# Kernel optimization log

Hardware: AMD Instinct MI355X
Metric: run time of the kernel (lower is better)

## Reference

```python
import jax, jax.numpy as jnp
import numpy as np

TEMP = 0.5
LAMDA = 1.0
NUM_SLICE = 64
EPS = 1e-20


def _gaussian_kernel(size=11, sigma=1.5):
    coords = np.arange(size, dtype=np.float64) - (size - 1) / 2.0
    g = np.exp(-(coords ** 2) / (2.0 * sigma ** 2))
    g = g / g.sum()
    return jnp.asarray(g, dtype=jnp.float32)


def _ssim(x, y, data_range=1.0, win_size=11, sigma=1.5):
    # x, y: [B, S, H, W]; treat each slice as an independent 1-channel image.
    B, S, H, W = x.shape
    x4 = x.reshape(B * S, 1, H, W)
    y4 = y.reshape(B * S, 1, H, W)
    g = _gaussian_kernel(win_size, sigma)
    kh = g.reshape(1, 1, win_size, 1)
    kw = g.reshape(1, 1, 1, win_size)
    dn = ('NCHW', 'OIHW', 'NCHW')

    def blur(a):
        a = jax.lax.conv_general_dilated(a, kh, (1, 1), 'VALID', dimension_numbers=dn)
        a = jax.lax.conv_general_dilated(a, kw, (1, 1), 'VALID', dimension_numbers=dn)
        return a

    mu1 = blur(x4)
    mu2 = blur(y4)
    mu1_sq = mu1 * mu1
    mu2_sq = mu2 * mu2
    mu1_mu2 = mu1 * mu2
    sigma1_sq = blur(x4 * x4) - mu1_sq
    sigma2_sq = blur(y4 * y4) - mu2_sq
    sigma12 = blur(x4 * y4) - mu1_mu2
    C1 = (0.01 * data_range) ** 2
    C2 = (0.03 * data_range) ** 2
    ssim_map = ((2.0 * mu1_mu2 + C1) * (2.0 * sigma12 + C2)) / (
        (mu1_sq + mu2_sq + C1) * (sigma1_sq + sigma2_sq + C2))
    return jnp.mean(ssim_map)


def _l1(a, b):
    return jnp.mean(jnp.abs(a - b))


def _cumulative_mips(img_fake, target, gumbel, temp):
    # Growing-window gumbel-softmax MIP, computed in a single O(S) pass.
    # softmax over a prefix window is shift-invariant, so subtract the
    # per-pixel global max over the slice axis for stability, then use cumsums.
    y = img_fake + gumbel
    m = jnp.max(y, axis=1, keepdims=True)
    e = jnp.exp((y - m) / temp)                      # unnormalized softmax weights
    num = jnp.cumsum(e * img_fake, axis=1)
    den = jnp.cumsum(e, axis=1)
    pred_c1 = num / den                              # prefix windows [0:idx+1]
    target_c1 = jax.lax.cummax(target, axis=1)

    ef = jnp.flip(e, axis=1)
    xf = jnp.flip(img_fake, axis=1)
    num2 = jnp.cumsum(ef * xf, axis=1)
    den2 = jnp.cumsum(ef, axis=1)
    pred_c2 = num2 / den2                            # suffix windows [S-1-idx:]
    target_c2 = jax.lax.cummax(jnp.flip(target, axis=1), axis=1)
    return pred_c1, target_c1, pred_c2, target_c2


def _forward(img_fake, target, u_noise):
    gumbel = -jnp.log(-jnp.log(u_noise + EPS) + EPS)
    p1, t1, p2, t2 = _cumulative_mips(img_fake, target, gumbel, TEMP)
    loss_lissim = (_l1(img_fake, target) + 1.0 - _ssim(img_fake, target)) * LAMDA
    loss_mip_c1 = (_l1(p1, t1) + 1.0 - _ssim(p1, t1)) * LAMDA
    loss_mip_c2 = (_l1(p2, t2) + 1.0 - _ssim(p2, t2)) * LAMDA
    return loss_lissim + loss_mip_c1 + loss_mip_c2


def setup_inputs() -> dict:
    key = jax.random.key(0)
    k1, k2, k3 = jax.random.split(key, 3)
    shape = (2, NUM_SLICE, 256, 256)
    img_fake = jax.random.uniform(k1, shape, dtype=jnp.float32)
    target = jax.random.uniform(k2, shape, dtype=jnp.float32)
    u_noise = jax.random.uniform(k3, shape, dtype=jnp.float32)
    return {"img_fake": img_fake, "target": target, "u_noise": u_noise}


def reference(img_fake, target, u_noise):
    return _forward(img_fake, target, u_noise)
```

## Files before the change

kernel.cpp:

```cpp
#include <hip/hip_runtime.h>
#include <cmath>
#include <cstring>

#define NUM_S   64
#define IMG_H   256
#define IMG_W   256
#define HWSZ    (IMG_H*IMG_W)
#define BATCH   2
#define NPIX    (BATCH*HWSZ)
#define NEL     (BATCH*NUM_S*HWSZ)
#define NSLICE  (BATCH*NUM_S)
#define VALID   246
#define EPS_F   1e-20f
#define C1_F    1e-4f
#define C2_F    9e-4f
#define RS      264
#define FS      (16*RS)
#define NSLOT_SCAN 1024
#define NSLOT_ALL  7168
#define PTPAD   1024

typedef __fp16 half8  __attribute__((ext_vector_type(8)));
typedef __fp16 fp16x2 __attribute__((ext_vector_type(2)));
using fragC = __attribute__((ext_vector_type(4))) float;

union H8 { half8 v; short s[8]; int i[4]; };
union PK { fp16x2 v; int i; };

struct GH { short h[11]; };

__device__ inline fp16x2 pkrtz(float a, float b) {
    return __builtin_amdgcn_cvt_pkrtz(a, b);
}
__device__ inline float frcp(float x)  { return __builtin_amdgcn_rcpf(x); }
__device__ inline float flog2(float x) { return __builtin_amdgcn_logf(x); }
__device__ inline float fexp2(float x) { return __builtin_amdgcn_exp2f(x); }

__device__ inline void block_reduce_slot(float v, float* slot) {
    __shared__ float sm[8];
    __syncthreads();
    #pragma unroll
    for (int off = 32; off; off >>= 1) v += __shfl_down(v, off, 64);
    int lane = threadIdx.x & 63, w = threadIdx.x >> 6;
    if (lane == 0) sm[w] = v;
    __syncthreads();
    if (threadIdx.x == 0) {
        float s = 0.f;
        int nw = blockDim.x >> 6;
        for (int i = 0; i < nw; ++i) s += sm[i];
        *slot = s;
    }
}

__global__ __launch_bounds__(256) void scan_kernel(
    const float* __restrict__ img, const float* __restrict__ tgt,
    const float* __restrict__ un,
    uint2* __restrict__ pt0, uint2* __restrict__ pt1, uint2* __restrict__ pt2,
    float* __restrict__ slots, GH gh, unsigned short* __restrict__ bandTbl)
{
    if (blockIdx.x == 0 && threadIdx.x < 64) {
        int q = threadIdx.x >> 4, n = threadIdx.x & 15;
        #pragma unroll
        for (int j = 0; j < 8; ++j) {
            int kk = q * 8 + j - n;
            short hv = 0;
            #pragma unroll
            for (int w = 0; w < 11; ++w) hv = (kk == w) ? gh.h[w] : hv;
            bandTbl[threadIdx.x * 8 + j] = (unsigned short)hv;
        }
    }

    const int HW2 = HWSZ / 2;
    int tid = blockIdx.x * 256 + threadIdx.x;
    bool bwd = tid >= (NPIX / 2);
    int p2 = bwd ? tid - NPIX / 2 : tid;
    int b   = p2 >> 15;
    int hw2 = p2 & (HW2 - 1);
    int idx  = b * (NUM_S * HW2) + hw2 + (bwd ? (NUM_S - 1) * HW2 : 0);
    int step = bwd ? -HW2 : HW2;
    const float2* __restrict__ img2 = (const float2*)img;
    const float2* __restrict__ tgt2 = (const float2*)tgt;
    const float2* __restrict__ un2  = (const float2*)un;

    float num[2] = {0.f, 0.f}, den[2] = {0.f, 0.f}, tm[2] = {-INFINITY, -INFINITY};
    float l1x = 0.f, l1p = 0.f;

    float2 xb[4], ub[4], tb[4];
    #pragma unroll
    for (int j = 0; j < 4; ++j) {
        int id = idx + j * step;
        xb[j] = img2[id]; ub[j] = un2[id]; tb[j] = tgt2[id];
    }

    for (int i = 0; i < NUM_S; i += 4) {
        #pragma unroll
        for (int j = 0; j < 4; ++j) {
            float2 x = xb[j], u = ub[j], t = tb[j];
            if (i + j + 4 < NUM_S) {
                int id = idx + 4 * step;
                xb[j] = img2[id]; ub[j] = un2[id]; tb[j] = tgt2[id];
            }
            float xc[2] = {x.x, x.y}, uc[2] = {u.x, u.y}, tc[2] = {t.x, t.y};
            float p[2];
            #pragma unroll
            for (int c = 0; c < 2; ++c) {
                float w = fmaf(flog2(uc[c] + EPS_F), -0.6931471805599453f, EPS_F);
                float r = frcp(w);
                float e = fexp2(xc[c] * 2.8853900817779268f) * (r * r);
                num[c] = fmaf(e, xc[c], num[c]);
                den[c] += e;
                p[c] = num[c] * frcp(den[c]);
                tm[c] = fmaxf(tm[c], tc[c]);
                if (!bwd) l1x += fabsf(xc[c] - tc[c]);
                l1p += fabsf(p[c] - tm[c]);
            }
            PK k0, k1;
            k0.v = pkrtz(p[0], tm[0]); k1.v = pkrtz(p[1], tm[1]);
            uint2 pv = make_uint2((unsigned)k0.i, (unsigned)k1.i);
            if (!bwd) {
                PK a0, a1;
                a0.v = pkrtz(xc[0], tc[0]); a1.v = pkrtz(xc[1], tc[1]);
                pt0[idx] = make_uint2((unsigned)a0.i, (unsigned)a1.i);
                pt1[idx] = pv;
            } else {
                pt2[idx] = pv;
            }
            idx += step;
        }
    }
    block_reduce_slot(bwd ? 0.f : l1x, &slots[blockIdx.x]);
    block_reduce_slot(l1p, &slots[512 + blockIdx.x]);
}

__global__ __launch_bounds__(256) void ssim_kernel(
    const unsigned* __restrict__ pt0, const unsigned* __restrict__ pt1,
    const unsigned* __restrict__ pt2,
    const int4* __restrict__ bandTbl, float* __restrict__ slots)
{
    __shared__ short Vl[5][FS];
    int pair  = blockIdx.z;
    int yy    = blockIdx.y;
    int bsel  = yy & 1, ss = yy >> 1;
    int sy    = bsel * NUM_S + ((pair == 2) ? ss : (NUM_S - 1 - ss));
    int base  = sy * HWSZ;
    int r0    = blockIdx.x * 16;
    int lane  = threadIdx.x & 63;
    int wid   = threadIdx.x >> 6;
    int q     = lane >> 4;
    int n     = lane & 15;

    const unsigned* __restrict__ pp =
        (pair == 0 ? pt0 : (pair == 1 ? pt1 : pt2)) + base;
    bool clampR = (r0 == 240);
    const fragC zero = {0.f, 0.f, 0.f, 0.f};

    unsigned ld[32];
    {
        int rowbase = r0 + q * 8;
        if (!clampR) {
            const unsigned* pb = pp + rowbase * IMG_W + n;
            #pragma unroll
            for (int it = 0; it < 4; ++it)
                #pragma unroll
                for (int j = 0; j < 8; ++j)
                    ld[it * 8 + j] = pb[j * IMG_W + (wid * 4 + it) * 16];
        } else {
            #pragma unroll
            for (int it = 0; it < 4; ++it)
                #pragma unroll
                for (int j = 0; j < 8; ++j) {
                    int rr = min(rowbase + j, IMG_H - 1);
                    ld[it * 8 + j] = pp[rr * IMG_W + (wid * 4 + it) * 16 + n];
                }
        }
    }
    H8 band;
    *(int4*)band.i = bandTbl[lane];

    for (int d = threadIdx.x; d < 320; d += 256) {
        int f = d >> 6, rm = d & 63, r = rm >> 2, cc = rm & 3;
        ((int*)Vl)[f * 2112 + r * 132 + 128 + cc] = 0;
    }

    #pragma unroll
    for (int it = 0; it < 4; ++it) {
        H8 fX, fY, fXX, fYY, fXY;
        #pragma unroll
        for (int j = 0; j < 4; ++j) {
            unsigned a = ld[it * 8 + 2 * j], b2 = ld[it * 8 + 2 * j + 1];
            fX.i[j] = (int)((a & 0xffffu) | (b2 << 16));
            fY.i[j] = (int)((a >> 16) | (b2 & 0xffff0000u));
        }
        fXX.v = fX.v * fX.v;
        fYY.v = fY.v * fY.v;
        fXY.v = fX.v * fY.v;
        fragC v0 = __builtin_amdgcn_mfma_f32_16x16x32_f16(fX.v,  band.v, zero, 0, 0, 0);
        fragC v1 = __builtin_amdgcn_mfma_f32_16x16x32_f16(fY.v,  band.v, zero, 0, 0, 0);
        fragC v2 = __builtin_amdgcn_mfma_f32_16x16x32_f16(fXX.v, band.v, zero, 0, 0, 0);
        fragC v3 = __builtin_amdgcn_mfma_f32_16x16x32_f16(fYY.v, band.v, zero, 0, 0, 0);
        fragC v4 = __builtin_amdgcn_mfma_f32_16x16x32_f16(fXY.v, band.v, zero, 0, 0, 0);
        int ro = n * RS + (wid * 4 + it) * 16 + q * 4;
        PK pa, pb;
        pa.v = pkrtz(v0[0], v0[1]); pb.v = pkrtz(v0[2], v0[3]);
        *(int2*)&Vl[0][ro] = make_int2(pa.i, pb.i);
        pa.v = pkrtz(v1[0], v1[1]); pb.v = pkrtz(v1[2], v1[3]);
        *(int2*)&Vl[1][ro] = make_int2(pa.i, pb.i);
        pa.v = pkrtz(v2[0], v2[1]); pb.v = pkrtz(v2[2], v2[3]);
        *(int2*)&Vl[2][ro] = make_int2(pa.i, pb.i);
        pa.v = pkrtz(v3[0], v3[1]); pb.v = pkrtz(v3[2], v3[3]);
        *(int2*)&Vl[3][ro] = make_int2(pa.i, pb.i);
        pa.v = pkrtz(v4[0], v4[1]); pb.v = pkrtz(v4[2], v4[3]);
        *(int2*)&Vl[4][ro] = make_int2(pa.i, pb.i);
    }
    __syncthreads();

    float lsum = 0.f;
    for (int it = 0; it < 4; ++it) {
        int c0 = (wid * 4 + it) * 16;
        int so = n * RS + c0 + q * 8;
        so = min(so, FS - 8);
        H8 a0, a1, a2, a3, a4;
        *(int4*)a0.i = *(const int4*)&Vl[0][so];
        *(int4*)a1.i = *(const int4*)&Vl[1][so];
        *(int4*)a2.i = *(const int4*)&Vl[2][so];
        *(int4*)a3.i = *(const int4*)&Vl[3][so];
        *(int4*)a4.i = *(const int4*)&Vl[4][so];
        fragC o0 = __builtin_amdgcn_mfma_f32_16x16x32_f16(a0.v, band.v, zero, 0, 0, 0);
        fragC o1 = __builtin_amdgcn_mfma_f32_16x16x32_f16(a1.v, band.v, zero, 0, 0, 0);
        fragC o2 = __builtin_amdgcn_mfma_f32_16x16x32_f16(a2.v, band.v, zero, 0, 0, 0);
        fragC o3 = __builtin_amdgcn_mfma_f32_16x16x32_f16(a3.v, band.v, zero, 0, 0, 0);
        fragC o4 = __builtin_amdgcn_mfma_f32_16x16x32_f16(a4.v, band.v, zero, 0, 0, 0);
        #pragma unroll
        for (int reg = 0; reg < 4; ++reg) {
            int r = r0 + q * 4 + reg;
            int c = c0 + n;
            if (r < VALID && c < VALID) {
                float m1 = o0[reg], m2 = o1[reg];
                float s11 = o2[reg] - m1 * m1;
                float s22 = o3[reg] - m2 * m2;
                float s12 = o4[reg] - m1 * m2;
                float nv = (2.f * m1 * m2 + C1_F) * (2.f * s12 + C2_F);
                float dv = (m1 * m1 + m2 * m2 + C1_F) * (s11 + s22 + C2_F);
                lsum += nv * frcp(dv);
            }
        }
    }
    block_reduce_slot(lsum,
        &slots[NSLOT_SCAN + pair * 2048 + blockIdx.y * 16 + blockIdx.x]);
}

__global__ void finalize_kernel(const float* __restrict__ slots,
                                float* __restrict__ out) {
    __shared__ double sa[4], sb[4];
    double a = 0.0, bsum = 0.0;
    for (int i = threadIdx.x; i < NSLOT_SCAN; i += 256) a += (double)slots[i];
    for (int i = NSLOT_SCAN + threadIdx.x; i < NSLOT_ALL; i += 256) bsum += (double)slots[i];
    #pragma unroll
    for (int off = 32; off; off >>= 1) {
        a    += __shfl_down(a, off, 64);
        bsum += __shfl_down(bsum, off, 64);
    }
    int lane = threadIdx.x & 63, w = threadIdx.x >> 6;
    if (lane == 0) { sa[w] = a; sb[w] = bsum; }
    __syncthreads();
    if (threadIdx.x == 0) {
        double A = sa[0] + sa[1] + sa[2] + sa[3];
        double B = sb[0] + sb[1] + sb[2] + sb[3];
        out[0] = (float)(3.0 + A / (double)NEL -
                         B / ((double)NSLICE * (double)VALID * (double)VALID));
    }
}

static unsigned short f32_to_f16(float f) {
    unsigned u; memcpy(&u, &f, 4);
    unsigned s = (u >> 16) & 0x8000u;
    int e = (int)((u >> 23) & 0xff) - 127 + 15;
    unsigned m = u & 0x7fffffu;
    unsigned h = s | ((unsigned)e << 10) | (m >> 13);
    unsigned rem = m & 0x1fffu;
    if (rem > 0x1000u || (rem == 0x1000u && (h & 1))) h++;
    return (unsigned short)h;
}
static double f16_to_d(unsigned short h) {
    unsigned e = (h >> 10) & 0x1f, m = h & 0x3ffu;
    return ldexp((double)(m + 1024), (int)e - 25);
}

extern "C" void kernel_launch(void* const* d_in, const int* in_sizes, int n_in,
                              void* d_out, int out_size, void* d_ws, size_t ws_size,
                              hipStream_t stream) {
    const float* img = (const float*)d_in[0];
    const float* tgt = (const float*)d_in[1];
    const float* un  = (const float*)d_in[2];
    float* out = (float*)d_out;

    unsigned* pt0 = (unsigned*)d_ws;
    unsigned* pt1 = pt0 + NEL + PTPAD;
    unsigned* pt2 = pt1 + NEL + PTPAD;
    float* slots = (float*)(pt2 + NEL);
    unsigned short* bandTbl = (unsigned short*)(slots + NSLOT_ALL);

    GH gh;
    {
        double g[11], s = 0.0;
        for (int i = 0; i < 11; ++i) { double d = i - 5; g[i] = exp(-d * d / 4.5); s += g[i]; }
        for (int i = 0; i < 11; ++i) g[i] /= s;
        for (int iter = 0; iter < 3; ++iter) {
            double sb = 0.0;
            unsigned short h[11];
            for (int i = 0; i < 11; ++i) { h[i] = f32_to_f16((float)g[i]); sb += f16_to_d(h[i]); }
            for (int i = 0; i < 11; ++i) { g[i] /= sb; gh.h[i] = (short)h[i]; }
        }
    }

    scan_kernel<<<NPIX / 256, 256, 0, stream>>>(img, tgt, un,
        (uint2*)pt0, (uint2*)pt1, (uint2*)pt2, slots, gh, bandTbl);
    ssim_kernel<<<dim3(16, NSLICE, 3), 256, 0, stream>>>(pt0, pt1, pt2,
        (const int4*)bandTbl, slots);
    finalize_kernel<<<1, 256, 0, stream>>>(slots, out);
}
```

Baseline: 193.3 us.

## Fuse scan and first SSIM pair into one launch, drop pt0 intermediate

The prefix-scan work and the SSIM of the raw image/target pair now run in one kernel as separate block ranges. The raw pair's SSIM reads fp32 inputs directly and converts them to fp16 in registers, so the packed pt0 buffer is neither written nor re-read. The band table is now built on the host and copied asynchronously, and the unpacking in the remaining SSIM kernel uses byte-permute instructions. This saves global traffic and some of the scan kernel's tail, but adds a host-to-device copy per call and mixes heterogeneous blocks in one grid.

New measurement: 196.2 us. Within noise of the previous version (+1.5%).

```diff
diff --git a/kernel.cpp b/kernel.cpp
--- a/kernel.cpp
+++ b/kernel.cpp
@@ -27,8 +27,6 @@
 union H8 { half8 v; short s[8]; int i[4]; };
 union PK { fp16x2 v; int i; };
 
-struct GH { short h[11]; };
-
 __device__ inline fp16x2 pkrtz(float a, float b) {
     return __builtin_amdgcn_cvt_pkrtz(a, b);
 }
@@ -52,168 +50,34 @@
     }
 }
 
-__global__ __launch_bounds__(256) void scan_kernel(
-    const float* __restrict__ img, const float* __restrict__ tgt,
-    const float* __restrict__ un,
-    uint2* __restrict__ pt0, uint2* __restrict__ pt1, uint2* __restrict__ pt2,
-    float* __restrict__ slots, GH gh, unsigned short* __restrict__ bandTbl)
-{
-    if (blockIdx.x == 0 && threadIdx.x < 64) {
-        int q = threadIdx.x >> 4, n = threadIdx.x & 15;
-        #pragma unroll
-        for (int j = 0; j < 8; ++j) {
-            int kk = q * 8 + j - n;
-            short hv = 0;
-            #pragma unroll
-            for (int w = 0; w < 11; ++w) hv = (kk == w) ? gh.h[w] : hv;
-            bandTbl[threadIdx.x * 8 + j] = (unsigned short)hv;
-        }
-    }
-
-    const int HW2 = HWSZ / 2;
-    int tid = blockIdx.x * 256 + threadIdx.x;
-    bool bwd = tid >= (NPIX / 2);
-    int p2 = bwd ? tid - NPIX / 2 : tid;
-    int b   = p2 >> 15;
-    int hw2 = p2 & (HW2 - 1);
-    int idx  = b * (NUM_S * HW2) + hw2 + (bwd ? (NUM_S - 1) * HW2 : 0);
-    int step = bwd ? -HW2 : HW2;
-    const float2* __restrict__ img2 = (const float2*)img;
-    const float2* __restrict__ tgt2 = (const float2*)tgt;
-    const float2* __restrict__ un2  = (const float2*)un;
-
-    float num[2] = {0.f, 0.f}, den[2] = {0.f, 0.f}, tm[2] = {-INFINITY, -INFINITY};
-    float l1x = 0.f, l1p = 0.f;
-
-    float2 xb[4], ub[4], tb[4];
-    #pragma unroll
-    for (int j = 0; j < 4; ++j) {
-        int id = idx + j * step;
-        xb[j] = img2[id]; ub[j] = un2[id]; tb[j] = tgt2[id];
-    }
-
-    for (int i = 0; i < NUM_S; i += 4) {
-        #pragma unroll
-        for (int j = 0; j < 4; ++j) {
-            float2 x = xb[j], u = ub[j], t = tb[j];
-            if (i + j + 4 < NUM_S) {
-                int id = idx + 4 * step;
-                xb[j] = img2[id]; ub[j] = un2[id]; tb[j] = tgt2[id];
-            }
-            float xc[2] = {x.x, x.y}, uc[2] = {u.x, u.y}, tc[2] = {t.x, t.y};
-            float p[2];
-            #pragma unroll
-            for (int c = 0; c < 2; ++c) {
-                float w = fmaf(flog2(uc[c] + EPS_F), -0.6931471805599453f, EPS_F);
-                float r = frcp(w);
-                float e = fexp2(xc[c] * 2.8853900817779268f) * (r * r);
-                num[c] = fmaf(e, xc[c], num[c]);
-                den[c] += e;
-                p[c] = num[c] * frcp(den[c]);
-                tm[c] = fmaxf(tm[c], tc[c]);
-                if (!bwd) l1x += fabsf(xc[c] - tc[c]);
-                l1p += fabsf(p[c] - tm[c]);
-            }
-            PK k0, k1;
-            k0.v = pkrtz(p[0], tm[0]); k1.v = pkrtz(p[1], tm[1]);
-            uint2 pv = make_uint2((unsigned)k0.i, (unsigned)k1.i);
-            if (!bwd) {
-                PK a0, a1;
-                a0.v = pkrtz(xc[0], tc[0]); a1.v = pkrtz(xc[1], tc[1]);
-                pt0[idx] = make_uint2((unsigned)a0.i, (unsigned)a1.i);
-                pt1[idx] = pv;
-            } else {
-                pt2[idx] = pv;
-            }
-            idx += step;
-        }
-    }
-    block_reduce_slot(bwd ? 0.f : l1x, &slots[blockIdx.x]);
-    block_reduce_slot(l1p, &slots[512 + blockIdx.x]);
-}
-
-__global__ __launch_bounds__(256) void ssim_kernel(
-    const unsigned* __restrict__ pt0, const unsigned* __restrict__ pt1,
-    const unsigned* __restrict__ pt2,
-    const int4* __restrict__ bandTbl, float* __restrict__ slots)
-{
-    __shared__ short Vl[5][FS];
-    int pair  = blockIdx.z;
-    int yy    = blockIdx.y;
-    int bsel  = yy & 1, ss = yy >> 1;
-    int sy    = bsel * NUM_S + ((pair == 2) ? ss : (NUM_S - 1 - ss));
-    int base  = sy * HWSZ;
-    int r0    = blockIdx.x * 16;
-    int lane  = threadIdx.x & 63;
-    int wid   = threadIdx.x >> 6;
-    int q     = lane >> 4;
-    int n     = lane & 15;
-
-    const unsigned* __restrict__ pp =
-        (pair == 0 ? pt0 : (pair == 1 ? pt1 : pt2)) + base;
-    bool clampR = (r0 == 240);
+__device__ inline void ssim_core_store(const H8& fX, const H8& fY, const H8& band,
+                                       short (*Vl)[FS], int ro) {
     const fragC zero = {0.f, 0.f, 0.f, 0.f};
-
-    unsigned ld[32];
-    {
-        int rowbase = r0 + q * 8;
-        if (!clampR) {
-            const unsigned* pb = pp + rowbase * IMG_W + n;
-            #pragma unroll
-            for (int it = 0; it < 4; ++it)
-                #pragma unroll
-                for (int j = 0; j < 8; ++j)
-                    ld[it * 8 + j] = pb[j * IMG_W + (wid * 4 + it) * 16];
-        } else {
-            #pragma unroll
-            for (int it = 0; it < 4; ++it)
-                #pragma unroll
-                for (int j = 0; j < 8; ++j) {
-                    int rr = min(rowbase + j, IMG_H - 1);
-                    ld[it * 8 + j] = pp[rr * IMG_W + (wid * 4 + it) * 16 + n];
-                }
-        }
-    }
-    H8 band;
-    *(int4*)band.i = bandTbl[lane];
-
-    for (int d = threadIdx.x; d < 320; d += 256) {
-        int f = d >> 6, rm = d & 63, r = rm >> 2, cc = rm & 3;
-        ((int*)Vl)[f * 2112 + r * 132 + 128 + cc] = 0;
-    }
-
-    #pragma unroll
-    for (int it = 0; it < 4; ++it) {
-        H8 fX, fY, fXX, fYY, fXY;
-        #pragma unroll
-        for (int j = 0; j < 4; ++j) {
-            unsigned a = ld[it * 8 + 2 * j], b2 = ld[it * 8 + 2 * j + 1];
-            fX.i[j] = (int)((a & 0xffffu) | (b2 << 16));
-            fY.i[j] = (int)((a >> 16) | (b2 & 0xffff0000u));
-        }
-        fXX.v = fX.v * fX.v;
-        fYY.v = fY.v * fY.v;
-        fXY.v = fX.v * fY.v;
-        fragC v0 = __builtin_amdgcn_mfma_f32_16x16x32_f16(fX.v,  band.v, zero, 0, 0, 0);
-        fragC v1 = __builtin_amdgcn_mfma_f32_16x16x32_f16(fY.v,  band.v, zero, 0, 0, 0);
-        fragC v2 = __builtin_amdgcn_mfma_f32_16x16x32_f16(fXX.v, band.v, zero, 0, 0, 0);
-        fragC v3 = __builtin_amdgcn_mfma_f32_16x16x32_f16(fYY.v, band.v, zero, 0, 0, 0);
-        fragC v4 = __builtin_amdgcn_mfma_f32_16x16x32_f16(fXY.v, band.v, zero, 0, 0, 0);
-        int ro = n * RS + (wid * 4 + it) * 16 + q * 4;
-        PK pa, pb;
-        pa.v = pkrtz(v0[0], v0[1]); pb.v = pkrtz(v0[2], v0[3]);
-        *(int2*)&Vl[0][ro] = make_int2(pa.i, pb.i);
-        pa.v = pkrtz(v1[0], v1[1]); pb.v = pkrtz(v1[2], v1[3]);
-        *(int2*)&Vl[1][ro] = make_int2(pa.i, pb.i);
-        pa.v = pkrtz(v2[0], v2[1]); pb.v = pkrtz(v2[2], v2[3]);
-        *(int2*)&Vl[2][ro] = make_int2(pa.i, pb.i);
-        pa.v = pkrtz(v3[0], v3[1]); pb.v = pkrtz(v3[2], v3[3]);
-        *(int2*)&Vl[3][ro] = make_int2(pa.i, pb.i);
-        pa.v = pkrtz(v4[0], v4[1]); pb.v = pkrtz(v4[2], v4[3]);
-        *(int2*)&Vl[4][ro] = make_int2(pa.i, pb.i);
-    }
-    __syncthreads();
-
+    H8 fXX, fYY, fXY;
+    fXX.v = fX.v * fX.v;
+    fYY.v = fY.v * fY.v;
+    fXY.v = fX.v * fY.v;
+    fragC v0 = __builtin_amdgcn_mfma_f32_16x16x32_f16(fX.v,  band.v, zero, 0, 0, 0);
+    fragC v1 = __builtin_amdgcn_mfma_f32_16x16x32_f16(fY.v,  band.v, zero, 0, 0, 0);
+    fragC v2 = __builtin_amdgcn_mfma_f32_16x16x32_f16(fXX.v, band.v, zero, 0, 0, 0);
+    fragC v3 = __builtin_amdgcn_mfma_f32_16x16x32_f16(fYY.v, band.v, zero, 0, 0, 0);
+    fragC v4 = __builtin_amdgcn_mfma_f32_16x16x32_f16(fXY.v, band.v, zero, 0, 0, 0);
+    PK pa, pb;
+    pa.v = pkrtz(v0[0], v0[1]); pb.v = pkrtz(v0[2], v0[3]);
+    *(int2*)&Vl[0][ro] = make_int2(pa.i, pb.i);
+    pa.v = pkrtz(v1[0], v1[1]); pb.v = pkrtz(v1[2], v1[3]);
+    *(int2*)&Vl[1][ro] = make_int2(pa.i, pb.i);
+    pa.v = pkrtz(v2[0], v2[1]); pb.v = pkrtz(v2[2], v2[3]);
+    *(int2*)&Vl[2][ro] = make_int2(pa.i, pb.i);
+    pa.v = pkrtz(v3[0], v3[1]); pb.v = pkrtz(v3[2], v3[3]);
+    *(int2*)&Vl[3][ro] = make_int2(pa.i, pb.i);
+    pa.v = pkrtz(v4[0], v4[1]); pb.v = pkrtz(v4[2], v4[3]);
+    *(int2*)&Vl[4][ro] = make_int2(pa.i, pb.i);
+}
+
+__device__ inline float ssim_stage2(short (*Vl)[FS], const H8& band,
+                                    int r0, int wid, int q, int n) {
+    const fragC zero = {0.f, 0.f, 0.f, 0.f};
     float lsum = 0.f;
     for (int it = 0; it < 4; ++it) {
         int c0 = (wid * 4 + it) * 16;
@@ -245,6 +109,191 @@
             }
         }
     }
+    return lsum;
+}
+
+__global__ __launch_bounds__(256) void fused_kernel(
+    const float* __restrict__ img, const float* __restrict__ tgt,
+    const float* __restrict__ un,
+    uint2* __restrict__ pt1, uint2* __restrict__ pt2,
+    const int4* __restrict__ bandTbl, float* __restrict__ slots)
+{
+    __shared__ short Vl[5][FS];
+    int bid = blockIdx.x;
+
+    if (bid < 512) {
+        const int HW2 = HWSZ / 2;
+        int tid = bid * 256 + threadIdx.x;
+        bool bwd = tid >= (NPIX / 2);
+        int p2 = bwd ? tid - NPIX / 2 : tid;
+        int b   = p2 >> 15;
+        int hw2 = p2 & (HW2 - 1);
+        int idx  = b * (NUM_S * HW2) + hw2 + (bwd ? (NUM_S - 1) * HW2 : 0);
+        int step = bwd ? -HW2 : HW2;
+        const float2* __restrict__ img2 = (const float2*)img;
+        const float2* __restrict__ tgt2 = (const float2*)tgt;
+        const float2* __restrict__ un2  = (const float2*)un;
+        uint2* __restrict__ pt = bwd ? pt2 : pt1;
+
+        float num[2] = {0.f, 0.f}, den[2] = {0.f, 0.f};
+        float tm[2] = {-INFINITY, -INFINITY};
+        float l1x = 0.f, l1p = 0.f;
+
+        float2 xb[4], ub[4], tb[4];
+        #pragma unroll
+        for (int j = 0; j < 4; ++j) {
+            int id = idx + j * step;
+            xb[j] = img2[id]; ub[j] = un2[id]; tb[j] = tgt2[id];
+        }
+
+        for (int i = 0; i < NUM_S; i += 4) {
+            #pragma unroll
+            for (int j = 0; j < 4; ++j) {
+                float2 x = xb[j], u = ub[j], t = tb[j];
+                if (i + j + 4 < NUM_S) {
+                    int id = idx + 4 * step;
+                    xb[j] = img2[id]; ub[j] = un2[id]; tb[j] = tgt2[id];
+                }
+                float xc[2] = {x.x, x.y}, uc[2] = {u.x, u.y}, tc[2] = {t.x, t.y};
+                float p[2];
+                #pragma unroll
+                for (int c = 0; c < 2; ++c) {
+                    float w = fmaf(flog2(uc[c] + EPS_F), -0.6931471805599453f, EPS_F);
+                    float r = frcp(w);
+                    float e = fexp2(xc[c] * 2.8853900817779268f) * (r * r);
+                    num[c] = fmaf(e, xc[c], num[c]);
+                    den[c] += e;
+                    p[c] = num[c] * frcp(den[c]);
+                    tm[c] = fmaxf(tm[c], tc[c]);
+                    if (!bwd) l1x += fabsf(xc[c] - tc[c]);
+                    l1p += fabsf(p[c] - tm[c]);
+                }
+                PK k0, k1;
+                k0.v = pkrtz(p[0], tm[0]); k1.v = pkrtz(p[1], tm[1]);
+                pt[idx] = make_uint2((unsigned)k0.i, (unsigned)k1.i);
+                idx += step;
+            }
+        }
+        block_reduce_slot(bwd ? 0.f : l1x, &slots[bid]);
+        block_reduce_slot(l1p, &slots[512 + bid]);
+        return;
+    }
+
+    int bi   = bid - 512;
+    int bx   = bi & 15, sy = bi >> 4;
+    int base = sy * HWSZ;
+    int r0   = bx * 16;
+    int lane = threadIdx.x & 63;
+    int wid  = threadIdx.x >> 6;
+    int q    = lane >> 4;
+    int n    = lane & 15;
+
+    H8 band;
+    *(int4*)band.i = bandTbl[lane];
+
+    for (int d = threadIdx.x; d < 320; d += 256) {
+        int f = d >> 6, rm = d & 63, r = rm >> 2, cc = rm & 3;
+        ((int*)Vl)[f * 2112 + r * 132 + 128 + cc] = 0;
+    }
+
+    bool clampR = (r0 == 240);
+    const float* __restrict__ pa = img + base;
+    const float* __restrict__ pb = tgt + base;
+    int rowbase = r0 + q * 8;
+    #pragma unroll
+    for (int it = 0; it < 4; ++it) {
+        int colb = (wid * 4 + it) * 16 + n;
+        float xv[8], yv[8];
+        if (!clampR) {
+            #pragma unroll
+            for (int j = 0; j < 8; ++j) {
+                xv[j] = pa[(rowbase + j) * IMG_W + colb];
+                yv[j] = pb[(rowbase + j) * IMG_W + colb];
+            }
+        } else {
+            #pragma unroll
+            for (int j = 0; j < 8; ++j) {
+                int rr = min(rowbase + j, IMG_H - 1);
+                xv[j] = pa[rr * IMG_W + colb];
+                yv[j] = pb[rr * IMG_W + colb];
+            }
+        }
+        H8 fX, fY;
+        #pragma unroll
+        for (int j = 0; j < 4; ++j) {
+            PK ka, kb;
+            ka.v = pkrtz(xv[2 * j], xv[2 * j + 1]); fX.i[j] = ka.i;
+            kb.v = pkrtz(yv[2 * j], yv[2 * j + 1]); fY.i[j] = kb.i;
+        }
+        int ro = n * RS + (wid * 4 + it) * 16 + q * 4;
+        ssim_core_store(fX, fY, band, Vl, ro);
+    }
+    __syncthreads();
+    float lsum = ssim_stage2(Vl, band, r0, wid, q, n);
+    block_reduce_slot(lsum, &slots[NSLOT_SCAN + sy * 16 + bx]);
+}
+
+__global__ __launch_bounds__(256) void ssim_kernel(
+    const unsigned* __restrict__ pt1, const unsigned* __restrict__ pt2,
+    const int4* __restrict__ bandTbl, float* __restrict__ slots)
+{
+    __shared__ short Vl[5][FS];
+    int pair  = blockIdx.z + 1;
+    int yy    = blockIdx.y;
+    int bsel  = yy & 1, ss = yy >> 1;
+    int sy    = bsel * NUM_S + ((pair == 2) ? ss : (NUM_S - 1 - ss));
+    int base  = sy * HWSZ;
+    int r0    = blockIdx.x * 16;
+    int lane  = threadIdx.x & 63;
+    int wid   = threadIdx.x >> 6;
+    int q     = lane >> 4;
+    int n     = lane & 15;
+
+    const unsigned* __restrict__ pp = (pair == 1 ? pt1 : pt2) + base;
+    bool clampR = (r0 == 240);
+
+    unsigned ld[32];
+    {
+        int rowbase = r0 + q * 8;
+        if (!clampR) {
+            const unsigned* pb = pp + rowbase * IMG_W + n;
+            #pragma unroll
+            for (int it = 0; it < 4; ++it)
+                #pragma unroll
+                for (int j = 0; j < 8; ++j)
+                    ld[it * 8 + j] = pb[j * IMG_W + (wid * 4 + it) * 16];
+        } else {
+            #pragma unroll
+            for (int it = 0; it < 4; ++it)
+                #pragma unroll
+                for (int j = 0; j < 8; ++j) {
+                    int rr = min(rowbase + j, IMG_H - 1);
+                    ld[it * 8 + j] = pp[rr * IMG_W + (wid * 4 + it) * 16 + n];
+                }
+        }
+    }
+    H8 band;
+    *(int4*)band.i = bandTbl[lane];
+
+    for (int d = threadIdx.x; d < 320; d += 256) {
+        int f = d >> 6, rm = d & 63, r = rm >> 2, cc = rm & 3;
+        ((int*)Vl)[f * 2112 + r * 132 + 128 + cc] = 0;
+    }
+
+    #pragma unroll
+    for (int it = 0; it < 4; ++it) {
+        H8 fX, fY;
+        #pragma unroll
+        for (int j = 0; j < 4; ++j) {
+            unsigned a = ld[it * 8 + 2 * j], b2 = ld[it * 8 + 2 * j + 1];
+            fX.i[j] = (int)__builtin_amdgcn_perm(b2, a, 0x05040100u);
+            fY.i[j] = (int)__builtin_amdgcn_perm(b2, a, 0x07060302u);
+        }
+        int ro = n * RS + (wid * 4 + it) * 16 + q * 4;
+        ssim_core_store(fX, fY, band, Vl, ro);
+    }
+    __syncthreads();
+    float lsum = ssim_stage2(Vl, band, r0, wid, q, n);
     block_reduce_slot(lsum,
         &slots[NSLOT_SCAN + pair * 2048 + blockIdx.y * 16 + blockIdx.x]);
 }
@@ -294,28 +343,35 @@
     const float* un  = (const float*)d_in[2];
     float* out = (float*)d_out;
 
-    unsigned* pt0 = (unsigned*)d_ws;
-    unsigned* pt1 = pt0 + NEL + PTPAD;
+    unsigned* pt1 = (unsigned*)d_ws;
     unsigned* pt2 = pt1 + NEL + PTPAD;
     float* slots = (float*)(pt2 + NEL);
     unsigned short* bandTbl = (unsigned short*)(slots + NSLOT_ALL);
 
-    GH gh;
+    static unsigned short h_band[64 * 8];
     {
         double g[11], s = 0.0;
+        unsigned short h[11];
         for (int i = 0; i < 11; ++i) { double d = i - 5; g[i] = exp(-d * d / 4.5); s += g[i]; }
         for (int i = 0; i < 11; ++i) g[i] /= s;
         for (int iter = 0; iter < 3; ++iter) {
             double sb = 0.0;
-            unsigned short h[11];
             for (int i = 0; i < 11; ++i) { h[i] = f32_to_f16((float)g[i]); sb += f16_to_d(h[i]); }
-            for (int i = 0; i < 11; ++i) { g[i] /= sb; gh.h[i] = (short)h[i]; }
-        }
-    }
-
-    scan_kernel<<<NPIX / 256, 256, 0, stream>>>(img, tgt, un,
-        (uint2*)pt0, (uint2*)pt1, (uint2*)pt2, slots, gh, bandTbl);
-    ssim_kernel<<<dim3(16, NSLICE, 3), 256, 0, stream>>>(pt0, pt1, pt2,
+            for (int i = 0; i < 11; ++i) g[i] /= sb;
+        }
+        for (int lane = 0; lane < 64; ++lane) {
+            int q = lane >> 4, n = lane & 15;
+            for (int j = 0; j < 8; ++j) {
+                int kk = q * 8 + j - n;
+                h_band[lane * 8 + j] = (kk >= 0 && kk < 11) ? h[kk] : 0;
+            }
+        }
+    }
+    hipMemcpyAsync(bandTbl, h_band, sizeof(h_band), hipMemcpyHostToDevice, stream);
+
+    fused_kernel<<<512 + 2048, 256, 0, stream>>>(img, tgt, un,
+        (uint2*)pt1, (uint2*)pt2, (const int4*)bandTbl, slots);
+    ssim_kernel<<<dim3(16, NSLICE, 2), 256, 0, stream>>>(pt1, pt2,
         (const int4*)bandTbl, slots);
     finalize_kernel<<<1, 256, 0, stream>>>(slots, out);
 }
```
